# Performance work log

Hardware: AMD Instinct MI355X
Metric: run time of the kernel (lower is better)

The kernel has to match this reference:

```python
import jax, jax.numpy as jnp
import numpy as np

BETA = 1.0 / np.sqrt(768.0).astype(np.float32)


def setup_inputs() -> dict:
    key = jax.random.key(0)
    k1, k2, k3 = jax.random.split(key, 3)
    x = jax.random.normal(k1, (32, 512, 768), dtype=jnp.float32)
    # torch nn.Linear(dim, n_prototype).weight has shape [n_prototype, dim]
    w_lookup = jax.random.normal(k2, (4096, 768), dtype=jnp.float32) * 0.02
    # torch nn.Linear(n_prototype, dim).weight has shape [dim, n_prototype]
    w_content = jax.random.normal(k3, (768, 4096), dtype=jnp.float32) * 0.02
    return {"x": x, "w_lookup": w_lookup, "w_content": w_content}


def reference(x, w_lookup, w_content):
    # scores: [b, s, n_prototype] = x @ w_lookup^T, scaled by 1/sqrt(dim)
    scores = jnp.einsum("bsd,pd->bsp", x, w_lookup) * jnp.asarray(BETA, x.dtype)
    lookup = jax.nn.softmax(scores, axis=-1)
    # content: [b, s, dim] = lookup @ w_content^T
    content = jnp.einsum("bsp,dp->bsd", lookup, w_content)
    return content  # dropout is identity in eval / p=0.0
```

## Files before the change

### kernel.cpp

```cpp
#include <hip/hip_runtime.h>
#include <hip/hip_bf16.h>


#define NTOK   16384
#define DIM    768
#define NPROT  4096
#define BETA_F 0.03608439182428583f

typedef __bf16 bf16_t;
typedef __bf16 bf16x8 __attribute__((ext_vector_type(8)));
typedef float  floatx4 __attribute__((ext_vector_type(4)));

__device__ __forceinline__ void async_copy16(const bf16_t* g, void* l) {
  __builtin_amdgcn_global_load_lds(
      (__attribute__((address_space(1))) const void*)g,
      (__attribute__((address_space(3))) void*)l, 16, 0, 0);
}

__global__ __launch_bounds__(256) void cvt_all(
    const float* __restrict__ x, const float* __restrict__ wl,
    const float* __restrict__ wc, bf16_t* __restrict__ xb,
    bf16_t* __restrict__ wlb, bf16_t* __restrict__ wcb,
    int nx8, int nw8, int nc8) {
  int i = blockIdx.x * 256 + threadIdx.x;
  const float* in; bf16_t* out; int k;
  if (i < nx8)            { in = x;  out = xb;  k = i; }
  else if (i < nx8 + nw8) { in = wl; out = wlb; k = i - nx8; }
  else if (i < nx8 + nw8 + nc8) { in = wc; out = wcb; k = i - nx8 - nw8; }
  else return;
  const float4* in4 = (const float4*)in;
  float4 a = in4[2 * k], b = in4[2 * k + 1];
  bf16x8 o;
  o[0] = (bf16_t)a.x; o[1] = (bf16_t)a.y; o[2] = (bf16_t)a.z; o[3] = (bf16_t)a.w;
  o[4] = (bf16_t)b.x; o[5] = (bf16_t)b.y; o[6] = (bf16_t)b.z; o[7] = (bf16_t)b.w;
  ((bf16x8*)out)[k] = o;
}

template <int EPI>
__global__ __launch_bounds__(512, 2)
void gemm256(const bf16_t* __restrict__ A, const bf16_t* __restrict__ B,
             void* __restrict__ Cv, float* __restrict__ rowsum,
             const int K, const int N, const int nN) {
  __shared__ char lds[131072];

  const int tid = threadIdx.x;
  const int l   = tid & 63;
  const int w   = tid >> 6;
  const int wr  = w >> 2;
  const int wc  = w & 3;
  const int lr  = l & 15;
  const int lk  = (l >> 4) << 3;

  const int nwg   = gridDim.x;
  const int chunk = nwg >> 3;
  const int wg    = (blockIdx.x & 7) * chunk + (blockIdx.x >> 3);
  const int m0    = (wg / nN) * 256;
  const int n0    = (wg % nN) * 256;

  int aoff[2][2], boff[2][2];
#pragma unroll
  for (int h = 0; h < 2; ++h)
#pragma unroll
    for (int j = 0; j < 2; ++j) {
      const int s     = j * 8 + w;
      const int mfrag = h * 8 + (s >> 1);
      const int ks    = s & 1;
      aoff[h][j] = (m0 + mfrag * 16 + lr) * K + ks * 32 + lk;
      boff[h][j] = (n0 + mfrag * 16 + lr) * K + ks * 32 + lk;
    }

  auto stageA = [&](int slot, int kt, int h) {
#pragma unroll
    for (int j = 0; j < 2; ++j) {
      const int s  = j * 8 + w;
      const int sf = (h * 8 + (s >> 1)) * 2 + (s & 1);
      async_copy16(A + aoff[h][j] + kt * 64, lds + slot * 65536 + sf * 1024);
    }
  };
  auto stageB = [&](int slot, int kt, int h) {
#pragma unroll
    for (int j = 0; j < 2; ++j) {
      const int s  = j * 8 + w;
      const int sf = (h * 8 + (s >> 1)) * 2 + (s & 1);
      async_copy16(B + boff[h][j] + kt * 64,
                   lds + slot * 65536 + 32768 + sf * 1024);
    }
  };

  bf16x8 afA[2][2], afB[2][2];
  bf16x8 bg[4][2];

  auto loadAf = [&](bf16x8 (&dst)[2][2], int slot, int mq) {
#pragma unroll
    for (int q = 0; q < 2; ++q)
#pragma unroll
      for (int ks = 0; ks < 2; ++ks)
        dst[q][ks] = *(const bf16x8*)(lds + slot * 65536 +
                        ((4 * mq + 2 * q + wr) * 2 + ks) * 1024 + l * 16);
  };
  auto loadBg = [&](int slot) {
#pragma unroll
    for (int nt = 0; nt < 4; ++nt)
#pragma unroll
      for (int ks = 0; ks < 2; ++ks)
        bg[nt][ks] = *(const bf16x8*)(lds + slot * 65536 + 32768 +
                        ((nt * 4 + wc) * 2 + ks) * 1024 + l * 16);
  };

  const floatx4 z = {0.f, 0.f, 0.f, 0.f};
  floatx4 acc[8][4];
#pragma unroll
  for (int mt = 0; mt < 8; ++mt)
#pragma unroll
    for (int nt = 0; nt < 4; ++nt) acc[mt][nt] = z;

  auto mma = [&](const bf16x8 (&af)[2][2], int mq) {
    __builtin_amdgcn_s_setprio(1);
#pragma unroll
    for (int q = 0; q < 2; ++q)
#pragma unroll
      for (int nt = 0; nt < 4; ++nt)
#pragma unroll
        for (int ks = 0; ks < 2; ++ks)
          acc[2 * mq + q][nt] = __builtin_amdgcn_mfma_f32_16x16x32_bf16(
              af[q][ks], bg[nt][ks], acc[2 * mq + q][nt], 0, 0, 0);
    __builtin_amdgcn_s_setprio(0);
  };

#define BAR()    do { __builtin_amdgcn_s_barrier(); \
                      __builtin_amdgcn_sched_barrier(0); } while (0)
#define VM(n)    asm volatile("s_waitcnt vmcnt(" #n ")" ::: "memory")

  const int T = K >> 6;

  stageA(0, 0, 0); stageA(0, 0, 1); stageB(0, 0, 0); stageB(0, 0, 1);
  stageB(1, 1, 0); stageB(1, 1, 1); stageA(1, 1, 0);
  VM(6);
  BAR();
  loadAf(afA, 0, 0);
  loadBg(0);

#pragma unroll 1
  for (int x = 0; x + 3 < T; x += 2) {
    stageA(1, x + 1, 1);
    loadAf(afB, 0, 1);
    mma(afA, 0); BAR();
    stageB(0, x + 2, 0);
    loadAf(afA, 0, 2);
    mma(afB, 1); BAR();
    stageB(0, x + 2, 1);
    loadAf(afB, 0, 3);
    mma(afA, 2);
    VM(4);
    BAR();
    stageA(0, x + 2, 0);
    loadAf(afA, 1, 0);
    mma(afB, 3);
    loadBg(1);
    BAR();
    stageA(0, x + 2, 1);
    loadAf(afB, 1, 1);
    mma(afA, 0); BAR();
    stageB(1, x + 3, 0);
    loadAf(afA, 1, 2);
    mma(afB, 1); BAR();
    stageB(1, x + 3, 1);
    loadAf(afB, 1, 3);
    mma(afA, 2);
    VM(4);
    BAR();
    stageA(1, x + 3, 0);
    loadAf(afA, 0, 0);
    mma(afB, 3);
    loadBg(0);
    BAR();
  }

  stageA(1, T - 1, 1);
  loadAf(afB, 0, 1);
  mma(afA, 0); BAR();
  loadAf(afA, 0, 2);
  mma(afB, 1); BAR();
  loadAf(afB, 0, 3);
  mma(afA, 2);
  VM(0);
  BAR();
  loadAf(afA, 1, 0);
  mma(afB, 3);
  loadBg(1);
  BAR();
  loadAf(afB, 1, 1);
  mma(afA, 0); BAR();
  loadAf(afA, 1, 2);
  mma(afB, 1); BAR();
  loadAf(afB, 1, 3);
  mma(afA, 2); BAR();
  mma(afB, 3);

#undef BAR
#undef VM

  const int hi4 = (l >> 4) << 2;
  if (EPI == 0) {
    bf16_t* P = (bf16_t*)Cv;
#pragma unroll
    for (int mt = 0; mt < 8; ++mt) {
      const int row = m0 + (mt * 2 + wr) * 16 + hi4;
      float rs[4] = {0.f, 0.f, 0.f, 0.f};
#pragma unroll
      for (int nt = 0; nt < 4; ++nt) {
        const int col = n0 + (nt * 4 + wc) * 16 + lr;
#pragma unroll
        for (int i = 0; i < 4; ++i) {
          const float e = __expf(acc[mt][nt][i] * BETA_F);
          P[(row + i) * N + col] = (bf16_t)e;
          rs[i] += e;
        }
      }
#pragma unroll
      for (int i = 0; i < 4; ++i) {
        float s = rs[i];
        s += __shfl_xor(s, 1);
        s += __shfl_xor(s, 2);
        s += __shfl_xor(s, 4);
        s += __shfl_xor(s, 8);
        if (lr == 0) atomicAdd(&rowsum[row + i], s);
      }
    }
  } else {
    float* O = (float*)Cv;
#pragma unroll
    for (int mt = 0; mt < 8; ++mt) {
      const int row = m0 + (mt * 2 + wr) * 16 + hi4;
#pragma unroll
      for (int i = 0; i < 4; ++i) {
        const float inv = 1.0f / rowsum[row + i];
#pragma unroll
        for (int nt = 0; nt < 4; ++nt)
          O[(row + i) * N + n0 + (nt * 4 + wc) * 16 + lr] = acc[mt][nt][i] * inv;
      }
    }
  }
}

__global__ __launch_bounds__(256) void hopfield_fallback(
    const float* __restrict__ x, const float* __restrict__ wl,
    const float* __restrict__ wc, float* __restrict__ out) {
  __shared__ float  xs[8 * 768];
  __shared__ bf16_t ps[8 * 4096];
  __shared__ float  rs[8];
  const int tid = threadIdx.x;
  const int r0  = blockIdx.x * 8;
  if (tid < 8) rs[tid] = 0.f;
  for (int i = tid; i < 8 * 768; i += 256)
    xs[i] = x[(r0 + (i / 768)) * 768 + (i % 768)];
  __syncthreads();

  float lsum[8] = {0, 0, 0, 0, 0, 0, 0, 0};
  for (int p = tid; p < 4096; p += 256) {
    float s[8] = {0, 0, 0, 0, 0, 0, 0, 0};
    for (int d = 0; d < 768; ++d) {
      const float wv = wl[p * 768 + d];
#pragma unroll
      for (int r = 0; r < 8; ++r) s[r] += xs[r * 768 + d] * wv;
    }
#pragma unroll
    for (int r = 0; r < 8; ++r) {
      const float e = __expf(s[r] * BETA_F);
      ps[r * 4096 + p] = (bf16_t)e;
      lsum[r] += e;
    }
  }
#pragma unroll
  for (int r = 0; r < 8; ++r) atomicAdd(&rs[r], lsum[r]);
  __syncthreads();

  for (int d = tid; d < 768; d += 256) {
    float o[8] = {0, 0, 0, 0, 0, 0, 0, 0};
    for (int p = 0; p < 4096; ++p) {
      const float wv = wc[d * 4096 + p];
#pragma unroll
      for (int r = 0; r < 8; ++r) o[r] += (float)ps[r * 4096 + p] * wv;
    }
#pragma unroll
    for (int r = 0; r < 8; ++r) out[(r0 + r) * 768 + d] = o[r] / rs[r];
  }
}

extern "C" void kernel_launch(void* const* d_in, const int* in_sizes, int n_in,
                              void* d_out, int out_size, void* d_ws, size_t ws_size,
                              hipStream_t stream) {
  (void)in_sizes; (void)n_in; (void)out_size;
  const float* x  = (const float*)d_in[0];
  const float* wl = (const float*)d_in[1];
  const float* wc = (const float*)d_in[2];
  float* out = (float*)d_out;

  const size_t xb_e = (size_t)NTOK * DIM;
  const size_t wl_e = (size_t)NPROT * DIM;
  const size_t wc_e = (size_t)DIM * NPROT;
  const size_t P_e  = (size_t)NTOK * NPROT;
  const size_t need = (xb_e + wl_e + wc_e + P_e) * 2 + (size_t)NTOK * 4;

  if (ws_size >= need) {
    char* ws = (char*)d_ws;
    bf16_t* xb  = (bf16_t*)ws;  ws += xb_e * 2;
    bf16_t* wlb = (bf16_t*)ws;  ws += wl_e * 2;
    bf16_t* wcb = (bf16_t*)ws;  ws += wc_e * 2;
    bf16_t* P   = (bf16_t*)ws;  ws += P_e * 2;
    float* rowsum = (float*)ws;

    hipMemsetAsync(rowsum, 0, NTOK * sizeof(float), stream);
    const int nx8 = (int)(xb_e / 8), nw8 = (int)(wl_e / 8), nc8 = (int)(wc_e / 8);
    cvt_all<<<(nx8 + nw8 + nc8 + 255) / 256, 256, 0, stream>>>(
        x, wl, wc, xb, wlb, wcb, nx8, nw8, nc8);
    gemm256<0><<<dim3((NTOK / 256) * (NPROT / 256)), 512, 0, stream>>>(
        xb, wlb, (void*)P, rowsum, DIM, NPROT, NPROT / 256);
    gemm256<1><<<dim3((NTOK / 256) * (DIM / 256)), 512, 0, stream>>>(
        P, wcb, (void*)out, rowsum, NPROT, DIM, DIM / 256);
  } else {
    hopfield_fallback<<<NTOK / 8, 256, 0, stream>>>(x, wl, wc, out);
  }
}
```

Before: 435.8 us.

## Switch GEMM to 32x32x16 MFMA tiles with simplified two-slot pipeline

Replaces 16x16x32 bf16 MFMAs with 32x32x16 MFMAs, giving each wave a contiguous 128x64 subtile held as 4x2 floatx16 accumulators. LDS fragment addressing is reworked to feed the larger instruction from the existing staged layout, and the hand-interleaved half-tile staging schedule is replaced by a simpler per-k-tile loop with explicit lgkmcnt waits. The epilogues are remapped to the 32x32 output layout, with a wider shuffle reduction for the softmax row sums. The larger MFMA shape needs fewer LDS fragment reads per FLOP, but the new schedule waits on LDS loads before each MFMA group, which may expose more latency.

```diff
diff --git a/kernel.cpp b/kernel.cpp
--- a/kernel.cpp
+++ b/kernel.cpp
@@ -9,7 +9,7 @@
 
 typedef __bf16 bf16_t;
 typedef __bf16 bf16x8 __attribute__((ext_vector_type(8)));
-typedef float  floatx4 __attribute__((ext_vector_type(4)));
+typedef float  floatx16 __attribute__((ext_vector_type(16)));
 
 __device__ __forceinline__ void async_copy16(const bf16_t* g, void* l) {
   __builtin_amdgcn_global_load_lds(
@@ -50,6 +50,8 @@
   const int wc  = w & 3;
   const int lr  = l & 15;
   const int lk  = (l >> 4) << 3;
+  const int l31 = l & 31;
+  const int h5  = l >> 5;
 
   const int nwg   = gridDim.x;
   const int chunk = nwg >> 3;
@@ -69,175 +71,177 @@
       boff[h][j] = (n0 + mfrag * 16 + lr) * K + ks * 32 + lk;
     }
 
-  auto stageA = [&](int slot, int kt, int h) {
-#pragma unroll
-    for (int j = 0; j < 2; ++j) {
-      const int s  = j * 8 + w;
-      const int sf = (h * 8 + (s >> 1)) * 2 + (s & 1);
-      async_copy16(A + aoff[h][j] + kt * 64, lds + slot * 65536 + sf * 1024);
-    }
-  };
-  auto stageB = [&](int slot, int kt, int h) {
-#pragma unroll
-    for (int j = 0; j < 2; ++j) {
-      const int s  = j * 8 + w;
-      const int sf = (h * 8 + (s >> 1)) * 2 + (s & 1);
-      async_copy16(B + boff[h][j] + kt * 64,
-                   lds + slot * 65536 + 32768 + sf * 1024);
-    }
-  };
-
-  bf16x8 afA[2][2], afB[2][2];
-  bf16x8 bg[4][2];
-
-  auto loadAf = [&](bf16x8 (&dst)[2][2], int slot, int mq) {
+  auto stageA32 = [&](int slot, int kt) {
+#pragma unroll
+    for (int h = 0; h < 2; ++h)
+#pragma unroll
+      for (int j = 0; j < 2; ++j) {
+        const int s  = j * 8 + w;
+        const int sf = (h * 8 + (s >> 1)) * 2 + (s & 1);
+        async_copy16(A + aoff[h][j] + kt * 64, lds + slot * 65536 + sf * 1024);
+      }
+  };
+  auto stageB32 = [&](int slot, int kt) {
+#pragma unroll
+    for (int h = 0; h < 2; ++h)
+#pragma unroll
+      for (int j = 0; j < 2; ++j) {
+        const int s  = j * 8 + w;
+        const int sf = (h * 8 + (s >> 1)) * 2 + (s & 1);
+        async_copy16(B + boff[h][j] + kt * 64,
+                     lds + slot * 65536 + 32768 + sf * 1024);
+      }
+  };
+
+  auto ldA = [&](int slot, int fm, int ks16) -> bf16x8 {
+    const int row = wr * 128 + fm * 32 + l31;
+    const int c   = ks16 * 2 + h5;
+    return *(const bf16x8*)(lds + slot * 65536 +
+               (((row >> 4) * 2 + (c >> 2)) << 10) +
+               (((row & 15) + ((c & 3) << 4)) << 4));
+  };
+  auto ldB = [&](int slot, int fn, int ks16) -> bf16x8 {
+    const int row = wc * 64 + fn * 32 + l31;
+    const int c   = ks16 * 2 + h5;
+    return *(const bf16x8*)(lds + slot * 65536 + 32768 +
+               (((row >> 4) * 2 + (c >> 2)) << 10) +
+               (((row & 15) + ((c & 3) << 4)) << 4));
+  };
+
+  bf16x8 af[2][4], bg[2][4];
+
+  const floatx16 z = {0.f};
+  floatx16 acc[4][2];
+#pragma unroll
+  for (int fm = 0; fm < 4; ++fm)
+#pragma unroll
+    for (int fn = 0; fn < 2; ++fn) acc[fm][fn] = z;
+
+  auto loadAfPair = [&](int slot, int mq) {
 #pragma unroll
     for (int q = 0; q < 2; ++q)
 #pragma unroll
-      for (int ks = 0; ks < 2; ++ks)
-        dst[q][ks] = *(const bf16x8*)(lds + slot * 65536 +
-                        ((4 * mq + 2 * q + wr) * 2 + ks) * 1024 + l * 16);
-  };
-  auto loadBg = [&](int slot) {
-#pragma unroll
-    for (int nt = 0; nt < 4; ++nt)
-#pragma unroll
-      for (int ks = 0; ks < 2; ++ks)
-        bg[nt][ks] = *(const bf16x8*)(lds + slot * 65536 + 32768 +
-                        ((nt * 4 + wc) * 2 + ks) * 1024 + l * 16);
-  };
-
-  const floatx4 z = {0.f, 0.f, 0.f, 0.f};
-  floatx4 acc[8][4];
-#pragma unroll
-  for (int mt = 0; mt < 8; ++mt)
-#pragma unroll
-    for (int nt = 0; nt < 4; ++nt) acc[mt][nt] = z;
-
-  auto mma = [&](const bf16x8 (&af)[2][2], int mq) {
+      for (int ks = 0; ks < 4; ++ks) af[q][ks] = ldA(slot, mq * 2 + q, ks);
+  };
+  auto loadBgAll = [&](int slot) {
+#pragma unroll
+    for (int fn = 0; fn < 2; ++fn)
+#pragma unroll
+      for (int ks = 0; ks < 4; ++ks) bg[fn][ks] = ldB(slot, fn, ks);
+  };
+
+  auto mma = [&](int mq) {
     __builtin_amdgcn_s_setprio(1);
 #pragma unroll
     for (int q = 0; q < 2; ++q)
 #pragma unroll
-      for (int nt = 0; nt < 4; ++nt)
-#pragma unroll
-        for (int ks = 0; ks < 2; ++ks)
-          acc[2 * mq + q][nt] = __builtin_amdgcn_mfma_f32_16x16x32_bf16(
-              af[q][ks], bg[nt][ks], acc[2 * mq + q][nt], 0, 0, 0);
+      for (int fn = 0; fn < 2; ++fn)
+#pragma unroll
+        for (int ks = 0; ks < 4; ++ks)
+          acc[mq * 2 + q][fn] = __builtin_amdgcn_mfma_f32_32x32x16_bf16(
+              af[q][ks], bg[fn][ks], acc[mq * 2 + q][fn], 0, 0, 0);
     __builtin_amdgcn_s_setprio(0);
   };
 
 #define BAR()    do { __builtin_amdgcn_s_barrier(); \
                       __builtin_amdgcn_sched_barrier(0); } while (0)
+#define LGKM0()  do { asm volatile("s_waitcnt lgkmcnt(0)" ::: "memory"); \
+                      __builtin_amdgcn_sched_barrier(0); } while (0)
 #define VM(n)    asm volatile("s_waitcnt vmcnt(" #n ")" ::: "memory")
 
   const int T = K >> 6;
 
-  stageA(0, 0, 0); stageA(0, 0, 1); stageB(0, 0, 0); stageB(0, 0, 1);
-  stageB(1, 1, 0); stageB(1, 1, 1); stageA(1, 1, 0);
-  VM(6);
+  stageA32(0, 0); stageB32(0, 0); stageB32(1, 1);
+  VM(4);
   BAR();
-  loadAf(afA, 0, 0);
-  loadBg(0);
 
 #pragma unroll 1
-  for (int x = 0; x + 3 < T; x += 2) {
-    stageA(1, x + 1, 1);
-    loadAf(afB, 0, 1);
-    mma(afA, 0); BAR();
-    stageB(0, x + 2, 0);
-    loadAf(afA, 0, 2);
-    mma(afB, 1); BAR();
-    stageB(0, x + 2, 1);
-    loadAf(afB, 0, 3);
-    mma(afA, 2);
-    VM(4);
-    BAR();
-    stageA(0, x + 2, 0);
-    loadAf(afA, 1, 0);
-    mma(afB, 3);
-    loadBg(1);
-    BAR();
-    stageA(0, x + 2, 1);
-    loadAf(afB, 1, 1);
-    mma(afA, 0); BAR();
-    stageB(1, x + 3, 0);
-    loadAf(afA, 1, 2);
-    mma(afB, 1); BAR();
-    stageB(1, x + 3, 1);
-    loadAf(afB, 1, 3);
-    mma(afA, 2);
-    VM(4);
-    BAR();
-    stageA(1, x + 3, 0);
-    loadAf(afA, 0, 0);
-    mma(afB, 3);
-    loadBg(0);
-    BAR();
-  }
-
-  stageA(1, T - 1, 1);
-  loadAf(afB, 0, 1);
-  mma(afA, 0); BAR();
-  loadAf(afA, 0, 2);
-  mma(afB, 1); BAR();
-  loadAf(afB, 0, 3);
-  mma(afA, 2);
+  for (int y = 0; y + 3 < T; y += 2) {
+#pragma unroll
+    for (int u = 0; u < 2; ++u) {
+      const int p = u;
+      loadAfPair(p, 0);
+      loadBgAll(p);
+      stageA32(p ^ 1, y + u + 1);
+      BAR(); LGKM0();
+      mma(0);
+      BAR();
+      loadAfPair(p, 1);
+      stageB32(p, y + u + 2);
+      BAR(); LGKM0();
+      mma(1);
+      VM(4);
+      BAR();
+    }
+  }
+
+  loadAfPair(0, 0);
+  loadBgAll(0);
+  stageA32(1, T - 1);
+  BAR(); LGKM0();
+  mma(0);
+  BAR();
+  loadAfPair(0, 1);
+  BAR(); LGKM0();
+  mma(1);
   VM(0);
   BAR();
-  loadAf(afA, 1, 0);
-  mma(afB, 3);
-  loadBg(1);
+  loadAfPair(1, 0);
+  loadBgAll(1);
+  BAR(); LGKM0();
+  mma(0);
   BAR();
-  loadAf(afB, 1, 1);
-  mma(afA, 0); BAR();
-  loadAf(afA, 1, 2);
-  mma(afB, 1); BAR();
-  loadAf(afB, 1, 3);
-  mma(afA, 2); BAR();
-  mma(afB, 3);
+  loadAfPair(1, 1);
+  BAR(); LGKM0();
+  mma(1);
 
 #undef BAR
+#undef LGKM0
 #undef VM
 
-  const int hi4 = (l >> 4) << 2;
   if (EPI == 0) {
     bf16_t* P = (bf16_t*)Cv;
 #pragma unroll
-    for (int mt = 0; mt < 8; ++mt) {
-      const int row = m0 + (mt * 2 + wr) * 16 + hi4;
-      float rs[4] = {0.f, 0.f, 0.f, 0.f};
-#pragma unroll
-      for (int nt = 0; nt < 4; ++nt) {
-        const int col = n0 + (nt * 4 + wc) * 16 + lr;
-#pragma unroll
-        for (int i = 0; i < 4; ++i) {
-          const float e = __expf(acc[mt][nt][i] * BETA_F);
-          P[(row + i) * N + col] = (bf16_t)e;
+    for (int fm = 0; fm < 4; ++fm) {
+      const int rowb = m0 + wr * 128 + fm * 32;
+      float rs[16];
+#pragma unroll
+      for (int i = 0; i < 16; ++i) rs[i] = 0.f;
+#pragma unroll
+      for (int fn = 0; fn < 2; ++fn) {
+        const int col = n0 + wc * 64 + fn * 32 + l31;
+#pragma unroll
+        for (int i = 0; i < 16; ++i) {
+          const float e = __expf(acc[fm][fn][i] * BETA_F);
+          const int row = rowb + (i & 3) + 8 * (i >> 2) + 4 * h5;
+          P[row * N + col] = (bf16_t)e;
           rs[i] += e;
         }
       }
 #pragma unroll
-      for (int i = 0; i < 4; ++i) {
+      for (int i = 0; i < 16; ++i) {
         float s = rs[i];
         s += __shfl_xor(s, 1);
         s += __shfl_xor(s, 2);
         s += __shfl_xor(s, 4);
         s += __shfl_xor(s, 8);
-        if (lr == 0) atomicAdd(&rowsum[row + i], s);
+        s += __shfl_xor(s, 16);
+        if (l31 == 0)
+          atomicAdd(&rowsum[rowb + (i & 3) + 8 * (i >> 2) + 4 * h5], s);
       }
     }
   } else {
     float* O = (float*)Cv;
 #pragma unroll
-    for (int mt = 0; mt < 8; ++mt) {
-      const int row = m0 + (mt * 2 + wr) * 16 + hi4;
-#pragma unroll
-      for (int i = 0; i < 4; ++i) {
-        const float inv = 1.0f / rowsum[row + i];
-#pragma unroll
-        for (int nt = 0; nt < 4; ++nt)
-          O[(row + i) * N + n0 + (nt * 4 + wc) * 16 + lr] = acc[mt][nt][i] * inv;
+    for (int fm = 0; fm < 4; ++fm) {
+      const int rowb = m0 + wr * 128 + fm * 32;
+#pragma unroll
+      for (int i = 0; i < 16; ++i) {
+        const int row = rowb + (i & 3) + 8 * (i >> 2) + 4 * h5;
+        const float inv = 1.0f / rowsum[row];
+#pragma unroll
+        for (int fn = 0; fn < 2; ++fn)
+          O[row * N + n0 + wc * 64 + fn * 32 + l31] = acc[fm][fn][i] * inv;
       }
     }
   }
```

Result: slower. 551.0 us (+26.4%).
